# Performance work log

Measured on AMD Instinct MI355X. Metric: run time of the kernel, lower is better.

## Reference

```python
import jax, jax.numpy as jnp
import numpy as np

N, FEAT, D, H, C, FF, PH, E = 50000, 64, 128, 4, 32, 512, 256, 600000
LN_EPS = 1e-5
NEG_SLOPE = 0.2


def layer_norm(x, g, b):
    m = x.mean(-1, keepdims=True)
    v = ((x - m) ** 2).mean(-1, keepdims=True)
    return (x - m) * jax.lax.rsqrt(v + LN_EPS) * g + b


def gat_conv(x, edge_index, W, a_src, a_dst, bias):
    # PyG GATConv, concat=True, add_self_loops=True, negative_slope=0.2, eval mode.
    n = x.shape[0]
    h = (x @ W).reshape(n, H, C)                       # [N,H,C]
    al_s = jnp.einsum('nhc,hc->nh', h, a_src)          # [N,H]
    al_d = jnp.einsum('nhc,hc->nh', h, a_dst)
    loops = jnp.arange(n)
    src = jnp.concatenate([edge_index[0], loops])      # [E+N]
    dst = jnp.concatenate([edge_index[1], loops])
    alpha = jax.nn.leaky_relu(al_s[src] + al_d[dst], NEG_SLOPE)  # [E+N,H]
    amax = jax.lax.stop_gradient(jax.ops.segment_max(alpha, dst, num_segments=n))
    ex = jnp.exp(alpha - amax[dst])
    denom = jax.ops.segment_sum(ex, dst, num_segments=n)
    w = ex / denom[dst]                                # segment softmax over incoming edges
    msg = h[src] * w[:, :, None]                       # [E+N,H,C]
    out = jax.ops.segment_sum(msg, dst, num_segments=n).reshape(n, H * C)
    return out + bias


def encoder_layer(x, ei, W, a_s, a_d, b, W1, b1, W2, b2, g1, bt1, g2, bt2):
    h = gat_conv(x, ei, W, a_s, a_d, b)
    x = layer_norm(x + h, g1, bt1)
    f = jax.nn.relu(x @ W1 + b1) @ W2 + b2
    return layer_norm(x + f, g2, bt2)


def setup_inputs() -> dict:
    key = jax.random.key(0)
    ks = iter(jax.random.split(key, 64))
    rn = lambda shp, s=0.08: jax.random.normal(next(ks), shp, dtype=jnp.float32) * s
    d = {}
    d['x'] = jax.random.normal(next(ks), (N, FEAT), dtype=jnp.float32)
    d['edge_index'] = jax.random.randint(next(ks), (2, E), 0, N)
    d['virtual_edge_index'] = jax.random.randint(next(ks), (2, E), 0, N)
    d['Wp'] = rn((FEAT, D)); d['bp'] = jnp.zeros((D,))
    d['lnp_g'] = jnp.ones((D,)); d['lnp_b'] = jnp.zeros((D,))
    for p in ('v', 'r'):
        d[p + 'W'] = rn((2, D, D)); d[p + '_as'] = rn((2, H, C), 0.1); d[p + '_ad'] = rn((2, H, C), 0.1)
        d[p + '_b'] = jnp.zeros((2, D))
        d[p + 'W1'] = rn((2, D, FF)); d[p + 'b1'] = jnp.zeros((2, FF))
        d[p + 'W2'] = rn((2, FF, D)); d[p + 'b2'] = jnp.zeros((2, D))
        d[p + 'ln1g'] = jnp.ones((2, D)); d[p + 'ln1b'] = jnp.zeros((2, D))
        d[p + 'ln2g'] = jnp.ones((2, D)); d[p + 'ln2b'] = jnp.zeros((2, D))
    d['We1'] = rn((2 * D, PH)); d['be1'] = jnp.zeros((PH,))
    d['We2'] = rn((PH, 1)); d['be2'] = jnp.zeros((1,))
    return d


def reference(x, edge_index, virtual_edge_index, Wp, bp, lnp_g, lnp_b,
              vW, v_as, v_ad, v_b, vW1, vb1, vW2, vb2, vln1g, vln1b, vln2g, vln2b,
              rW, r_as, r_ad, r_b, rW1, rb1, rW2, rb2, rln1g, rln1b, rln2g, rln2b,
              We1, be1, We2, be2):
    # preprocessing
    h = layer_norm(jax.nn.relu(x @ Wp + bp), lnp_g, lnp_b)
    # virtual-link encoders
    for i in range(vW.shape[0]):
        h = encoder_layer(h, virtual_edge_index, vW[i], v_as[i], v_ad[i], v_b[i],
                          vW1[i], vb1[i], vW2[i], vb2[i], vln1g[i], vln1b[i], vln2g[i], vln2b[i])
    # real-link encoders
    for i in range(rW.shape[0]):
        h = encoder_layer(h, edge_index, rW[i], r_as[i], r_ad[i], r_b[i],
                          rW1[i], rb1[i], rW2[i], rb2[i], rln1g[i], rln1b[i], rln2g[i], rln2b[i])
    # edge predictor
    ef = jnp.concatenate([h[edge_index[0]], h[edge_index[1]]], axis=-1)  # [E,2D]
    flow = (jax.nn.relu(ef @ We1 + be1) @ We2 + be2)[:, 0]
    return jax.nn.relu(flow)
```

## Files before the change

kernel.cpp:

```cpp
#include <hip/hip_runtime.h>
#include <hip/hip_bf16.h>
#include <math.h>

#define NODES 50000
#define NFEAT 64
#define DIM 128
#define HEADS 4
#define CHC 32
#define FFDIM 512
#define PHDIM 256
#define NEDGE 600000
#define LN_EPS 1e-5f
#define SLOPE 0.2f

typedef __attribute__((ext_vector_type(8))) short bf16x8;
typedef __attribute__((ext_vector_type(4))) float f32x4;
typedef __attribute__((ext_vector_type(4))) unsigned short us4;

__device__ __forceinline__ unsigned short f2bf(float f) {
    __hip_bfloat16 h = __float2bfloat16(f);
    return reinterpret_cast<unsigned short&>(h);
}
__device__ __forceinline__ float bf2f(unsigned short u) {
    return __uint_as_float(((unsigned int)u) << 16);
}

__device__ __forceinline__ void ln_stats128(float val, float* red, float& mean, float& rstd) {
    float s1 = val, s2 = val * val;
#pragma unroll
    for (int off = 32; off > 0; off >>= 1) {
        s1 += __shfl_xor(s1, off, 64);
        s2 += __shfl_xor(s2, off, 64);
    }
    int wv = threadIdx.x >> 6;
    if ((threadIdx.x & 63) == 0) { red[wv * 2] = s1; red[wv * 2 + 1] = s2; }
    __syncthreads();
    float t1 = red[0] + red[2];
    float t2 = red[1] + red[3];
    mean = t1 * (1.f / 128.f);
    float var = t2 * (1.f / 128.f) - mean * mean;
    rstd = rsqrtf(var + LN_EPS);
}

__global__ void k_count(const int* __restrict__ dst, int* __restrict__ cnt) {
    int e = blockIdx.x * 256 + threadIdx.x;
    if (e < NEDGE) atomicAdd(&cnt[dst[e]], 1);
}

__global__ void k_scan(const int* __restrict__ deg, int* __restrict__ rp) {
    __shared__ int sh[1024];
    int t = threadIdx.x;
    const int per = (NODES + 1023) / 1024;
    int beg = t * per;
    int end = beg + per; if (end > NODES) end = NODES; if (beg > NODES) beg = NODES;
    int s = 0;
    for (int i = beg; i < end; i++) s += deg[i];
    sh[t] = s;
    __syncthreads();
    for (int off = 1; off < 1024; off <<= 1) {
        int v = (t >= off) ? sh[t - off] : 0;
        __syncthreads();
        sh[t] += v;
        __syncthreads();
    }
    int run = sh[t] - s;
    for (int i = beg; i < end; i++) { rp[i] = run; run += deg[i]; }
    if (t == 1023) rp[NODES] = sh[1023];
}

__global__ void k_fill(const int* __restrict__ ei, const int* __restrict__ rp,
                       int* __restrict__ cnt, int* __restrict__ ci) {
    int e = blockIdx.x * 256 + threadIdx.x;
    if (e < NEDGE) {
        int s = ei[e], d = ei[NEDGE + e];
        int pos = atomicAdd(&cnt[d], 1);
        ci[rp[d] + pos] = s;
    }
}

template <int KI, int NR>
__global__ void k_wcvt2(const float* __restrict__ in, unsigned short* __restrict__ oh,
                        unsigned short* __restrict__ ol) {
    int tid = blockIdx.x * 256 + threadIdx.x;
    int n = tid / KI, k = tid % KI;
    float w = in[k * NR + n];
    unsigned short h = f2bf(w);
    oh[tid] = h;
    ol[tid] = f2bf(w - bf2f(h));
}

__global__ void k_preprocess(const float* __restrict__ x0, const float* __restrict__ Wp,
                             const float* __restrict__ bp, const float* __restrict__ g,
                             const float* __restrict__ b, float* __restrict__ xout) {
    __shared__ float xr[NFEAT];
    __shared__ float red[4];
    int n = blockIdx.x;
    int j = threadIdx.x;
    if (j < NFEAT) xr[j] = x0[n * NFEAT + j];
    __syncthreads();
    float acc = bp[j];
#pragma unroll
    for (int k = 0; k < NFEAT; k++) acc += xr[k] * Wp[k * DIM + j];
    acc = fmaxf(acc, 0.f);
    float mean, rstd;
    ln_stats128(acc, red, mean, rstd);
    xout[n * DIM + j] = (acc - mean) * rstd * g[j] + b[j];
}

#define XS_STRIDE 136
#define HID_STRIDE 520
#define FB_STRIDE 132
#define MFMA_BF16 __builtin_amdgcn_mfma_f32_16x16x32_bf16

__global__ void k_xw_mfma(const float* __restrict__ x,
                          const unsigned short* __restrict__ Wh,
                          const unsigned short* __restrict__ Wl,
                          const float* __restrict__ a_s, const float* __restrict__ a_d,
                          float* __restrict__ hg, float* __restrict__ als,
                          float* __restrict__ ald) {
    __shared__ __align__(16) unsigned short xsh[32 * XS_STRIDE];
    __shared__ __align__(16) unsigned short xsl[32 * XS_STRIDE];
    int t = threadIdx.x;
    int n0 = blockIdx.x * 32;

#pragma unroll
    for (int jj = 0; jj < 4; jj++) {
        int v = t + jj * 256;
        int m = v >> 5, c4 = (v & 31) * 4;
        int node = n0 + m;
        float4 f;
        if (node < NODES) f = *(const float4*)(x + (size_t)node * DIM + c4);
        else { f.x = f.y = f.z = f.w = 0.f; }
        us4 uh = {f2bf(f.x), f2bf(f.y), f2bf(f.z), f2bf(f.w)};
        us4 ul = {f2bf(f.x - bf2f(uh.x)), f2bf(f.y - bf2f(uh.y)),
                  f2bf(f.z - bf2f(uh.z)), f2bf(f.w - bf2f(uh.w))};
        *(us4*)(xsh + m * XS_STRIDE + c4) = uh;
        *(us4*)(xsl + m * XS_STRIDE + c4) = ul;
    }
    __syncthreads();

    int wv = t >> 6, l = t & 63, lr = l & 15, lk = l >> 4;

    f32x4 acc[2][2];
#pragma unroll
    for (int mf = 0; mf < 2; mf++)
#pragma unroll
        for (int nf = 0; nf < 2; nf++) acc[mf][nf] = (f32x4){0.f, 0.f, 0.f, 0.f};
#pragma unroll
    for (int kk = 0; kk < 4; kk++) {
        int c = kk * 32 + lk * 8;
        bf16x8 a0h = *(const bf16x8*)(xsh + lr * XS_STRIDE + c);
        bf16x8 a0l = *(const bf16x8*)(xsl + lr * XS_STRIDE + c);
        bf16x8 a1h = *(const bf16x8*)(xsh + (16 + lr) * XS_STRIDE + c);
        bf16x8 a1l = *(const bf16x8*)(xsl + (16 + lr) * XS_STRIDE + c);
#pragma unroll
        for (int nf = 0; nf < 2; nf++) {
            int n = wv * 32 + nf * 16 + lr;
            bf16x8 bh = *(const bf16x8*)(Wh + (size_t)n * DIM + c);
            bf16x8 bl = *(const bf16x8*)(Wl + (size_t)n * DIM + c);
            acc[0][nf] = MFMA_BF16(a0h, bh, acc[0][nf], 0, 0, 0);
            acc[0][nf] = MFMA_BF16(a0l, bh, acc[0][nf], 0, 0, 0);
            acc[0][nf] = MFMA_BF16(a0h, bl, acc[0][nf], 0, 0, 0);
            acc[1][nf] = MFMA_BF16(a1h, bh, acc[1][nf], 0, 0, 0);
            acc[1][nf] = MFMA_BF16(a1l, bh, acc[1][nf], 0, 0, 0);
            acc[1][nf] = MFMA_BF16(a1h, bl, acc[1][nf], 0, 0, 0);
        }
    }

    float as0 = a_s[wv * 32 + lr], as1 = a_s[wv * 32 + 16 + lr];
    float ad0 = a_d[wv * 32 + lr], ad1 = a_d[wv * 32 + 16 + lr];
#pragma unroll
    for (int mf = 0; mf < 2; mf++) {
#pragma unroll
        for (int r = 0; r < 4; r++) {
            int m = mf * 16 + lk * 4 + r;
            int node = n0 + m;
            float v0 = acc[mf][0][r], v1 = acc[mf][1][r];
            if (node < NODES) {
                hg[(size_t)node * DIM + wv * 32 + lr] = v0;
                hg[(size_t)node * DIM + wv * 32 + 16 + lr] = v1;
            }
            float ps = v0 * as0 + v1 * as1;
            float pd = v0 * ad0 + v1 * ad1;
#pragma unroll
            for (int off = 8; off > 0; off >>= 1) {
                ps += __shfl_xor(ps, off, 64);
                pd += __shfl_xor(pd, off, 64);
            }
            if (lr == 0 && node < NODES) {
                als[node * HEADS + wv] = ps;
                ald[node * HEADS + wv] = pd;
            }
        }
    }
}

__global__ void k_agg(const float* __restrict__ x, const float* __restrict__ hg,
                      const float* __restrict__ als, const float* __restrict__ ald,
                      const int* __restrict__ rp, const int* __restrict__ ci,
                      const float* __restrict__ bias, const float* __restrict__ g,
                      const float* __restrict__ b, float* __restrict__ y) {
    __shared__ float red[4];
    int n = blockIdx.x, j = threadIdx.x, head = j >> 5;
    float aldn = ald[n * HEADS + head];
    float a0 = als[n * HEADS + head] + aldn;
    a0 = (a0 > 0.f) ? a0 : SLOPE * a0;
    float ex = __expf(a0);
    float den = ex;
    float acc = ex * hg[(size_t)n * DIM + j];
    int beg = rp[n], end = rp[n + 1];
    int e = beg;
    for (; e + 4 <= end; e += 4) {
        int s0 = ci[e], s1 = ci[e + 1], s2 = ci[e + 2], s3 = ci[e + 3];
        float av0 = als[s0 * HEADS + head] + aldn;
        float av1 = als[s1 * HEADS + head] + aldn;
        float av2 = als[s2 * HEADS + head] + aldn;
        float av3 = als[s3 * HEADS + head] + aldn;
        av0 = (av0 > 0.f) ? av0 : SLOPE * av0;
        av1 = (av1 > 0.f) ? av1 : SLOPE * av1;
        av2 = (av2 > 0.f) ? av2 : SLOPE * av2;
        av3 = (av3 > 0.f) ? av3 : SLOPE * av3;
        float e0 = __expf(av0), e1 = __expf(av1), e2 = __expf(av2), e3 = __expf(av3);
        float h0 = hg[(size_t)s0 * DIM + j];
        float h1 = hg[(size_t)s1 * DIM + j];
        float h2 = hg[(size_t)s2 * DIM + j];
        float h3 = hg[(size_t)s3 * DIM + j];
        den += (e0 + e1) + (e2 + e3);
        acc += e0 * h0 + e1 * h1 + e2 * h2 + e3 * h3;
    }
    for (; e < end; e++) {
        int s = ci[e];
        float av = als[s * HEADS + head] + aldn;
        av = (av > 0.f) ? av : SLOPE * av;
        float e2 = __expf(av);
        den += e2;
        acc += e2 * hg[(size_t)s * DIM + j];
    }
    float val = x[(size_t)n * DIM + j] + acc / den + bias[j];
    float mean, rstd;
    ln_stats128(val, red, mean, rstd);
    y[(size_t)n * DIM + j] = (val - mean) * rstd * g[j] + b[j];
}

#define TM 32

__global__ void k_ffn_mfma(
    const float* __restrict__ yin,
    const unsigned short* __restrict__ W1h, const unsigned short* __restrict__ W1l,
    const float* __restrict__ b1,
    const unsigned short* __restrict__ W2h, const unsigned short* __restrict__ W2l,
    const float* __restrict__ b2, const float* __restrict__ g,
    const float* __restrict__ b, float* __restrict__ xout) {
    __shared__ __align__(16) unsigned char smem[(2 * TM * XS_STRIDE + 2 * TM * HID_STRIDE) * 2];
    unsigned short* xsh = (unsigned short*)smem;
    unsigned short* xsl = xsh + TM * XS_STRIDE;
    unsigned short* hidh = xsl + TM * XS_STRIDE;
    unsigned short* hidl = hidh + TM * HID_STRIDE;
    float* fbuf = (float*)hidh;

    int t = threadIdx.x;
    int n0 = blockIdx.x * TM;

#pragma unroll
    for (int jj = 0; jj < 2; jj++) {
        int v = t + jj * 512;
        int m = v >> 5, c4 = (v & 31) * 4;
        int node = n0 + m;
        float4 f;
        if (node < NODES) f = *(const float4*)(yin + (size_t)node * DIM + c4);
        else { f.x = f.y = f.z = f.w = 0.f; }
        us4 uh = {f2bf(f.x), f2bf(f.y), f2bf(f.z), f2bf(f.w)};
        us4 ul = {f2bf(f.x - bf2f(uh.x)), f2bf(f.y - bf2f(uh.y)),
                  f2bf(f.z - bf2f(uh.z)), f2bf(f.w - bf2f(uh.w))};
        *(us4*)(xsh + m * XS_STRIDE + c4) = uh;
        *(us4*)(xsl + m * XS_STRIDE + c4) = ul;
    }
    __syncthreads();

    int wv = t >> 6, l = t & 63, lr = l & 15, lk = l >> 4;

    {
        f32x4 acc[2][4];
#pragma unroll
        for (int mf = 0; mf < 2; mf++)
#pragma unroll
            for (int nf = 0; nf < 4; nf++) acc[mf][nf] = (f32x4){0.f, 0.f, 0.f, 0.f};
#pragma unroll
        for (int kk = 0; kk < 4; kk++) {
            int c = kk * 32 + lk * 8;
            bf16x8 a0h = *(const bf16x8*)(xsh + lr * XS_STRIDE + c);
            bf16x8 a0l = *(const bf16x8*)(xsl + lr * XS_STRIDE + c);
            bf16x8 a1h = *(const bf16x8*)(xsh + (16 + lr) * XS_STRIDE + c);
            bf16x8 a1l = *(const bf16x8*)(xsl + (16 + lr) * XS_STRIDE + c);
#pragma unroll
            for (int nf = 0; nf < 4; nf++) {
                int n = wv * 64 + nf * 16 + lr;
                bf16x8 bh = *(const bf16x8*)(W1h + (size_t)n * DIM + c);
                bf16x8 bl = *(const bf16x8*)(W1l + (size_t)n * DIM + c);
                acc[0][nf] = MFMA_BF16(a0h, bh, acc[0][nf], 0, 0, 0);
                acc[0][nf] = MFMA_BF16(a0l, bh, acc[0][nf], 0, 0, 0);
                acc[0][nf] = MFMA_BF16(a0h, bl, acc[0][nf], 0, 0, 0);
                acc[1][nf] = MFMA_BF16(a1h, bh, acc[1][nf], 0, 0, 0);
                acc[1][nf] = MFMA_BF16(a1l, bh, acc[1][nf], 0, 0, 0);
                acc[1][nf] = MFMA_BF16(a1h, bl, acc[1][nf], 0, 0, 0);
            }
        }
#pragma unroll
        for (int nf = 0; nf < 4; nf++) {
            int n = wv * 64 + nf * 16 + lr;
            float bias = b1[n];
#pragma unroll
            for (int mf = 0; mf < 2; mf++)
#pragma unroll
                for (int r = 0; r < 4; r++) {
                    int m = mf * 16 + lk * 4 + r;
                    float val = fmaxf(acc[mf][nf][r] + bias, 0.f);
                    unsigned short h = f2bf(val);
                    hidh[m * HID_STRIDE + n] = h;
                    hidl[m * HID_STRIDE + n] = f2bf(val - bf2f(h));
                }
        }
    }
    __syncthreads();

    f32x4 acc2[2];
#pragma unroll
    for (int mf = 0; mf < 2; mf++) acc2[mf] = (f32x4){0.f, 0.f, 0.f, 0.f};
#pragma unroll
    for (int kk = 0; kk < 16; kk++) {
        int c = kk * 32 + lk * 8;
        bf16x8 a0h = *(const bf16x8*)(hidh + lr * HID_STRIDE + c);
        bf16x8 a0l = *(const bf16x8*)(hidl + lr * HID_STRIDE + c);
        bf16x8 a1h = *(const bf16x8*)(hidh + (16 + lr) * HID_STRIDE + c);
        bf16x8 a1l = *(const bf16x8*)(hidl + (16 + lr) * HID_STRIDE + c);
        int n = wv * 16 + lr;
        bf16x8 bh = *(const bf16x8*)(W2h + (size_t)n * FFDIM + c);
        bf16x8 bl = *(const bf16x8*)(W2l + (size_t)n * FFDIM + c);
        acc2[0] = MFMA_BF16(a0h, bh, acc2[0], 0, 0, 0);
        acc2[0] = MFMA_BF16(a0l, bh, acc2[0], 0, 0, 0);
        acc2[0] = MFMA_BF16(a0h, bl, acc2[0], 0, 0, 0);
        acc2[1] = MFMA_BF16(a1h, bh, acc2[1], 0, 0, 0);
        acc2[1] = MFMA_BF16(a1l, bh, acc2[1], 0, 0, 0);
        acc2[1] = MFMA_BF16(a1h, bl, acc2[1], 0, 0, 0);
    }
    __syncthreads();

    {
        int n = wv * 16 + lr;
        float bias = b2[n];
#pragma unroll
        for (int mf = 0; mf < 2; mf++)
#pragma unroll
            for (int r = 0; r < 4; r++) {
                int m = mf * 16 + lk * 4 + r;
                int node = n0 + m;
                float yv = (node < NODES) ? yin[(size_t)node * DIM + n] : 0.f;
                fbuf[m * FB_STRIDE + n] = acc2[mf][r] + bias + yv;
            }
    }
    __syncthreads();

    {
        int row = t >> 4, l16 = t & 15;
        float4 vv[2];
        float s1 = 0.f, s2 = 0.f;
#pragma unroll
        for (int q = 0; q < 2; q++) {
            vv[q] = *(float4*)(fbuf + row * FB_STRIDE + l16 * 8 + q * 4);
            s1 += vv[q].x + vv[q].y + vv[q].z + vv[q].w;
            s2 += vv[q].x * vv[q].x + vv[q].y * vv[q].y + vv[q].z * vv[q].z + vv[q].w * vv[q].w;
        }
#pragma unroll
        for (int off = 8; off > 0; off >>= 1) {
            s1 += __shfl_xor(s1, off, 64);
            s2 += __shfl_xor(s2, off, 64);
        }
        float mean = s1 * (1.f / 128.f);
        float var = s2 * (1.f / 128.f) - mean * mean;
        float rstd = rsqrtf(var + LN_EPS);
        int node = n0 + row;
        if (node < NODES) {
#pragma unroll
            for (int q = 0; q < 2; q++) {
                int c = l16 * 8 + q * 4;
                float4 gv = *(const float4*)(g + c);
                float4 bv = *(const float4*)(b + c);
                float4 o;
                o.x = (vv[q].x - mean) * rstd * gv.x + bv.x;
                o.y = (vv[q].y - mean) * rstd * gv.y + bv.y;
                o.z = (vv[q].z - mean) * rstd * gv.z + bv.z;
                o.w = (vv[q].w - mean) * rstd * gv.w + bv.w;
                *(float4*)(xout + (size_t)node * DIM + c) = o;
            }
        }
    }
}

#define TF 16
__global__ void k_pq(const float* __restrict__ h, const float* __restrict__ We1,
                     const float* __restrict__ be1, __hip_bfloat16* __restrict__ P,
                     __hip_bfloat16* __restrict__ Q) {
    __shared__ float xs[TF][DIM];
    int n0 = blockIdx.x * TF;
    int t = threadIdx.x;
    for (int i = t; i < TF * DIM; i += 256) {
        int e = i >> 7, k = i & 127;
        xs[e][k] = h[(size_t)(n0 + e) * DIM + k];
    }
    __syncthreads();
    float accP[TF], accQ[TF];
#pragma unroll
    for (int e = 0; e < TF; e++) { accP[e] = be1[t]; accQ[e] = 0.f; }
    for (int k = 0; k < DIM; k++) {
        float wp = We1[k * PHDIM + t];
        float wq = We1[(DIM + k) * PHDIM + t];
#pragma unroll
        for (int e = 0; e < TF; e++) {
            float xv = xs[e][k];
            accP[e] += xv * wp;
            accQ[e] += xv * wq;
        }
    }
#pragma unroll
    for (int e = 0; e < TF; e++) {
        P[(size_t)(n0 + e) * PHDIM + t] = __float2bfloat16(accP[e]);
        Q[(size_t)(n0 + e) * PHDIM + t] = __float2bfloat16(accQ[e]);
    }
}

__global__ void k_edge(const int* __restrict__ ei, const __hip_bfloat16* __restrict__ P,
                       const __hip_bfloat16* __restrict__ Q, const float* __restrict__ We2,
                       const float* __restrict__ be2, float* __restrict__ out) {
    int lane = threadIdx.x & 63;
    int wv = threadIdx.x >> 6;
    int e = blockIdx.x * 4 + wv;
    if (e >= NEDGE) return;
    float4 w2 = ((const float4*)We2)[lane];
    int s = ei[e], d = ei[NEDGE + e];
    uint2 pu = ((const uint2*)P)[(size_t)s * 64 + lane];
    uint2 qu = ((const uint2*)Q)[(size_t)d * 64 + lane];
    float p0 = __uint_as_float(pu.x << 16);
    float p1 = __uint_as_float(pu.x & 0xffff0000u);
    float p2 = __uint_as_float(pu.y << 16);
    float p3 = __uint_as_float(pu.y & 0xffff0000u);
    float q0 = __uint_as_float(qu.x << 16);
    float q1 = __uint_as_float(qu.x & 0xffff0000u);
    float q2 = __uint_as_float(qu.y << 16);
    float q3 = __uint_as_float(qu.y & 0xffff0000u);
    float acc = fmaxf(p0 + q0, 0.f) * w2.x + fmaxf(p1 + q1, 0.f) * w2.y +
                fmaxf(p2 + q2, 0.f) * w2.z + fmaxf(p3 + q3, 0.f) * w2.w;
#pragma unroll
    for (int off = 32; off > 0; off >>= 1) acc += __shfl_xor(acc, off, 64);
    if (lane == 0) out[e] = fmaxf(acc + be2[0], 0.f);
}

extern "C" void kernel_launch(void* const* d_in, const int* in_sizes, int n_in,
                              void* d_out, int out_size, void* d_ws, size_t ws_size,
                              hipStream_t stream) {
    const float* x0   = (const float*)d_in[0];
    const int*   eiR  = (const int*)d_in[1];
    const int*   eiV  = (const int*)d_in[2];
    const float* Wp   = (const float*)d_in[3];
    const float* bp   = (const float*)d_in[4];
    const float* lnpg = (const float*)d_in[5];
    const float* lnpb = (const float*)d_in[6];
    const float* vW   = (const float*)d_in[7];
    const float* v_as = (const float*)d_in[8];
    const float* v_ad = (const float*)d_in[9];
    const float* v_b  = (const float*)d_in[10];
    const float* vW1  = (const float*)d_in[11];
    const float* vb1  = (const float*)d_in[12];
    const float* vW2  = (const float*)d_in[13];
    const float* vb2  = (const float*)d_in[14];
    const float* vln1g = (const float*)d_in[15];
    const float* vln1b = (const float*)d_in[16];
    const float* vln2g = (const float*)d_in[17];
    const float* vln2b = (const float*)d_in[18];
    const float* rW   = (const float*)d_in[19];
    const float* r_as = (const float*)d_in[20];
    const float* r_ad = (const float*)d_in[21];
    const float* r_b  = (const float*)d_in[22];
    const float* rW1  = (const float*)d_in[23];
    const float* rb1  = (const float*)d_in[24];
    const float* rW2  = (const float*)d_in[25];
    const float* rb2  = (const float*)d_in[26];
    const float* rln1g = (const float*)d_in[27];
    const float* rln1b = (const float*)d_in[28];
    const float* rln2g = (const float*)d_in[29];
    const float* rln2b = (const float*)d_in[30];
    const float* We1  = (const float*)d_in[31];
    const float* be1  = (const float*)d_in[32];
    const float* We2  = (const float*)d_in[33];
    const float* be2  = (const float*)d_in[34];
    float* out = (float*)d_out;

    float* X   = (float*)d_ws;
    float* Y   = X + (size_t)NODES * DIM;
    float* HG  = Y + (size_t)NODES * DIM;
    float* ALS = HG + (size_t)NODES * DIM;
    float* ALD = ALS + (size_t)NODES * HEADS;
    __hip_bfloat16* Pb = (__hip_bfloat16*)(ALD + (size_t)NODES * HEADS);
    __hip_bfloat16* Qb = Pb + (size_t)NODES * PHDIM;
    unsigned short* WT = (unsigned short*)(Qb + (size_t)NODES * PHDIM);
    unsigned short* WXT = WT + (size_t)4 * 4 * 65536;
    int* rpV = (int*)(WXT + (size_t)4 * 2 * 16384);
    int* ciV = rpV + (NODES + 1);
    int* rpR = ciV + NEDGE;
    int* ciR = rpR + (NODES + 1);
    int* cnt = ciR + NEDGE;

    const int EB = (NEDGE + 255) / 256;

    hipMemsetAsync(cnt, 0, sizeof(int) * NODES, stream);
    k_count<<<EB, 256, 0, stream>>>(eiV + NEDGE, cnt);
    k_scan<<<1, 1024, 0, stream>>>(cnt, rpV);
    hipMemsetAsync(cnt, 0, sizeof(int) * NODES, stream);
    k_fill<<<EB, 256, 0, stream>>>(eiV, rpV, cnt, ciV);
    hipMemsetAsync(cnt, 0, sizeof(int) * NODES, stream);
    k_count<<<EB, 256, 0, stream>>>(eiR + NEDGE, cnt);
    k_scan<<<1, 1024, 0, stream>>>(cnt, rpR);
    hipMemsetAsync(cnt, 0, sizeof(int) * NODES, stream);
    k_fill<<<EB, 256, 0, stream>>>(eiR, rpR, cnt, ciR);

    for (int l = 0; l < 4; l++) {
        bool virt = (l < 2);
        int i = virt ? l : (l - 2);
        const float* W1 = (virt ? vW1 : rW1) + (size_t)i * DIM * FFDIM;
        const float* W2 = (virt ? vW2 : rW2) + (size_t)i * FFDIM * DIM;
        const float* W  = (virt ? vW : rW) + (size_t)i * DIM * DIM;
        unsigned short* base = WT + (size_t)l * 262144;
        k_wcvt2<DIM, FFDIM><<<256, 256, 0, stream>>>(W1, base, base + 65536);
        k_wcvt2<FFDIM, DIM><<<256, 256, 0, stream>>>(W2, base + 131072, base + 196608);
        unsigned short* bx = WXT + (size_t)l * 32768;
        k_wcvt2<DIM, DIM><<<64, 256, 0, stream>>>(W, bx, bx + 16384);
    }

    k_preprocess<<<NODES, 128, 0, stream>>>(x0, Wp, bp, lnpg, lnpb, X);

    for (int l = 0; l < 4; l++) {
        bool virt = (l < 2);
        int i = virt ? l : (l - 2);
        const float* As = (virt ? v_as : r_as) + (size_t)i * HEADS * CHC;
        const float* Ad = (virt ? v_ad : r_ad) + (size_t)i * HEADS * CHC;
        const float* Bb = (virt ? v_b : r_b) + (size_t)i * DIM;
        const float* B1 = (virt ? vb1 : rb1) + (size_t)i * FFDIM;
        const float* B2 = (virt ? vb2 : rb2) + (size_t)i * DIM;
        const float* G1 = (virt ? vln1g : rln1g) + (size_t)i * DIM;
        const float* B1n = (virt ? vln1b : rln1b) + (size_t)i * DIM;
        const float* G2 = (virt ? vln2g : rln2g) + (size_t)i * DIM;
        const float* B2n = (virt ? vln2b : rln2b) + (size_t)i * DIM;
        const int* rp = virt ? rpV : rpR;
        const int* ci = virt ? ciV : ciR;

        unsigned short* bx = WXT + (size_t)l * 32768;
        k_xw_mfma<<<(NODES + 31) / 32, 256, 0, stream>>>(X, bx, bx + 16384, As, Ad, HG, ALS, ALD);
        k_agg<<<NODES, 128, 0, stream>>>(X, HG, ALS, ALD, rp, ci, Bb, G1, B1n, Y);
        unsigned short* base = WT + (size_t)l * 262144;
        k_ffn_mfma<<<(NODES + TM - 1) / TM, 512, 0, stream>>>(
            Y, base, base + 65536, B1, base + 131072, base + 196608, B2, G2, B2n, X);
    }

    k_pq<<<NODES / TF, 256, 0, stream>>>(X, We1, be1, Pb, Qb);
    k_edge<<<(NEDGE + 3) / 4, 256, 0, stream>>>(eiR, Pb, Qb, We2, be2, out);
}
```

Baseline: 1.424 ms.

## Split FFN tile rows across twice as many waves in k_ffn_mfma

The FFN kernel now launches 1024 threads per block instead of 512, and each wave computes one 16-row half of the 32-row tile instead of both halves. This halves per-wave accumulator state and MFMA work, which adds waves for latency hiding. In exchange, every global weight fragment (W1, W2) is loaded by twice as many waves per block. The larger block may also limit how many blocks fit per CU.

```diff
diff --git a/kernel.cpp b/kernel.cpp
--- a/kernel.cpp
+++ b/kernel.cpp
@@ -261,10 +261,8 @@
     int t = threadIdx.x;
     int n0 = blockIdx.x * TM;
 
-#pragma unroll
-    for (int jj = 0; jj < 2; jj++) {
-        int v = t + jj * 512;
-        int m = v >> 5, c4 = (v & 31) * 4;
+    {
+        int m = t >> 5, c4 = (t & 31) * 4;
         int node = n0 + m;
         float4 f;
         if (node < NODES) f = *(const float4*)(yin + (size_t)node * DIM + c4);
@@ -278,100 +276,79 @@
     __syncthreads();
 
     int wv = t >> 6, l = t & 63, lr = l & 15, lk = l >> 4;
+    int mh = (wv & 1) * 16;
+    int cg = wv >> 1;
 
     {
-        f32x4 acc[2][4];
-#pragma unroll
-        for (int mf = 0; mf < 2; mf++)
-#pragma unroll
-            for (int nf = 0; nf < 4; nf++) acc[mf][nf] = (f32x4){0.f, 0.f, 0.f, 0.f};
+        f32x4 acc[4];
+#pragma unroll
+        for (int nf = 0; nf < 4; nf++) acc[nf] = (f32x4){0.f, 0.f, 0.f, 0.f};
 #pragma unroll
         for (int kk = 0; kk < 4; kk++) {
             int c = kk * 32 + lk * 8;
-            bf16x8 a0h = *(const bf16x8*)(xsh + lr * XS_STRIDE + c);
-            bf16x8 a0l = *(const bf16x8*)(xsl + lr * XS_STRIDE + c);
-            bf16x8 a1h = *(const bf16x8*)(xsh + (16 + lr) * XS_STRIDE + c);
-            bf16x8 a1l = *(const bf16x8*)(xsl + (16 + lr) * XS_STRIDE + c);
+            bf16x8 ah = *(const bf16x8*)(xsh + (mh + lr) * XS_STRIDE + c);
+            bf16x8 al = *(const bf16x8*)(xsl + (mh + lr) * XS_STRIDE + c);
 #pragma unroll
             for (int nf = 0; nf < 4; nf++) {
-                int n = wv * 64 + nf * 16 + lr;
+                int n = cg * 64 + nf * 16 + lr;
                 bf16x8 bh = *(const bf16x8*)(W1h + (size_t)n * DIM + c);
                 bf16x8 bl = *(const bf16x8*)(W1l + (size_t)n * DIM + c);
-                acc[0][nf] = MFMA_BF16(a0h, bh, acc[0][nf], 0, 0, 0);
-                acc[0][nf] = MFMA_BF16(a0l, bh, acc[0][nf], 0, 0, 0);
-                acc[0][nf] = MFMA_BF16(a0h, bl, acc[0][nf], 0, 0, 0);
-                acc[1][nf] = MFMA_BF16(a1h, bh, acc[1][nf], 0, 0, 0);
-                acc[1][nf] = MFMA_BF16(a1l, bh, acc[1][nf], 0, 0, 0);
-                acc[1][nf] = MFMA_BF16(a1h, bl, acc[1][nf], 0, 0, 0);
+                acc[nf] = MFMA_BF16(ah, bh, acc[nf], 0, 0, 0);
+                acc[nf] = MFMA_BF16(al, bh, acc[nf], 0, 0, 0);
+                acc[nf] = MFMA_BF16(ah, bl, acc[nf], 0, 0, 0);
             }
         }
 #pragma unroll
         for (int nf = 0; nf < 4; nf++) {
-            int n = wv * 64 + nf * 16 + lr;
+            int n = cg * 64 + nf * 16 + lr;
             float bias = b1[n];
 #pragma unroll
-            for (int mf = 0; mf < 2; mf++)
-#pragma unroll
-                for (int r = 0; r < 4; r++) {
-                    int m = mf * 16 + lk * 4 + r;
-                    float val = fmaxf(acc[mf][nf][r] + bias, 0.f);
-                    unsigned short h = f2bf(val);
-                    hidh[m * HID_STRIDE + n] = h;
-                    hidl[m * HID_STRIDE + n] = f2bf(val - bf2f(h));
-                }
-        }
-    }
-    __syncthreads();
-
-    f32x4 acc2[2];
-#pragma unroll
-    for (int mf = 0; mf < 2; mf++) acc2[mf] = (f32x4){0.f, 0.f, 0.f, 0.f};
+            for (int r = 0; r < 4; r++) {
+                int m = mh + lk * 4 + r;
+                float val = fmaxf(acc[nf][r] + bias, 0.f);
+                unsigned short h = f2bf(val);
+                hidh[m * HID_STRIDE + n] = h;
+                hidl[m * HID_STRIDE + n] = f2bf(val - bf2f(h));
+            }
+        }
+    }
+    __syncthreads();
+
+    f32x4 acc2 = (f32x4){0.f, 0.f, 0.f, 0.f};
 #pragma unroll
     for (int kk = 0; kk < 16; kk++) {
         int c = kk * 32 + lk * 8;
-        bf16x8 a0h = *(const bf16x8*)(hidh + lr * HID_STRIDE + c);
-        bf16x8 a0l = *(const bf16x8*)(hidl + lr * HID_STRIDE + c);
-        bf16x8 a1h = *(const bf16x8*)(hidh + (16 + lr) * HID_STRIDE + c);
-        bf16x8 a1l = *(const bf16x8*)(hidl + (16 + lr) * HID_STRIDE + c);
-        int n = wv * 16 + lr;
+        bf16x8 ah = *(const bf16x8*)(hidh + (mh + lr) * HID_STRIDE + c);
+        bf16x8 al = *(const bf16x8*)(hidl + (mh + lr) * HID_STRIDE + c);
+        int n = cg * 16 + lr;
         bf16x8 bh = *(const bf16x8*)(W2h + (size_t)n * FFDIM + c);
         bf16x8 bl = *(const bf16x8*)(W2l + (size_t)n * FFDIM + c);
-        acc2[0] = MFMA_BF16(a0h, bh, acc2[0], 0, 0, 0);
-        acc2[0] = MFMA_BF16(a0l, bh, acc2[0], 0, 0, 0);
-        acc2[0] = MFMA_BF16(a0h, bl, acc2[0], 0, 0, 0);
-        acc2[1] = MFMA_BF16(a1h, bh, acc2[1], 0, 0, 0);
-        acc2[1] = MFMA_BF16(a1l, bh, acc2[1], 0, 0, 0);
-        acc2[1] = MFMA_BF16(a1h, bl, acc2[1], 0, 0, 0);
+        acc2 = MFMA_BF16(ah, bh, acc2, 0, 0, 0);
+        acc2 = MFMA_BF16(al, bh, acc2, 0, 0, 0);
+        acc2 = MFMA_BF16(ah, bl, acc2, 0, 0, 0);
     }
     __syncthreads();
 
     {
-        int n = wv * 16 + lr;
+        int n = cg * 16 + lr;
         float bias = b2[n];
 #pragma unroll
-        for (int mf = 0; mf < 2; mf++)
-#pragma unroll
-            for (int r = 0; r < 4; r++) {
-                int m = mf * 16 + lk * 4 + r;
-                int node = n0 + m;
-                float yv = (node < NODES) ? yin[(size_t)node * DIM + n] : 0.f;
-                fbuf[m * FB_STRIDE + n] = acc2[mf][r] + bias + yv;
-            }
+        for (int r = 0; r < 4; r++) {
+            int m = mh + lk * 4 + r;
+            int node = n0 + m;
+            float yv = (node < NODES) ? yin[(size_t)node * DIM + n] : 0.f;
+            fbuf[m * FB_STRIDE + n] = acc2[r] + bias + yv;
+        }
     }
     __syncthreads();
 
     {
-        int row = t >> 4, l16 = t & 15;
-        float4 vv[2];
-        float s1 = 0.f, s2 = 0.f;
-#pragma unroll
-        for (int q = 0; q < 2; q++) {
-            vv[q] = *(float4*)(fbuf + row * FB_STRIDE + l16 * 8 + q * 4);
-            s1 += vv[q].x + vv[q].y + vv[q].z + vv[q].w;
-            s2 += vv[q].x * vv[q].x + vv[q].y * vv[q].y + vv[q].z * vv[q].z + vv[q].w * vv[q].w;
-        }
-#pragma unroll
-        for (int off = 8; off > 0; off >>= 1) {
+        int row = t >> 5, l32 = t & 31;
+        float4 vv = *(float4*)(fbuf + row * FB_STRIDE + l32 * 4);
+        float s1 = vv.x + vv.y + vv.z + vv.w;
+        float s2 = vv.x * vv.x + vv.y * vv.y + vv.z * vv.z + vv.w * vv.w;
+#pragma unroll
+        for (int off = 16; off > 0; off >>= 1) {
             s1 += __shfl_xor(s1, off, 64);
             s2 += __shfl_xor(s2, off, 64);
         }
@@ -380,18 +357,15 @@
         float rstd = rsqrtf(var + LN_EPS);
         int node = n0 + row;
         if (node < NODES) {
-#pragma unroll
-            for (int q = 0; q < 2; q++) {
-                int c = l16 * 8 + q * 4;
-                float4 gv = *(const float4*)(g + c);
-                float4 bv = *(const float4*)(b + c);
-                float4 o;
-                o.x = (vv[q].x - mean) * rstd * gv.x + bv.x;
-                o.y = (vv[q].y - mean) * rstd * gv.y + bv.y;
-                o.z = (vv[q].z - mean) * rstd * gv.z + bv.z;
-                o.w = (vv[q].w - mean) * rstd * gv.w + bv.w;
-                *(float4*)(xout + (size_t)node * DIM + c) = o;
-            }
+            int c = l32 * 4;
+            float4 gv = *(const float4*)(g + c);
+            float4 bv = *(const float4*)(b + c);
+            float4 o;
+            o.x = (vv.x - mean) * rstd * gv.x + bv.x;
+            o.y = (vv.y - mean) * rstd * gv.y + bv.y;
+            o.z = (vv.z - mean) * rstd * gv.z + bv.z;
+            o.w = (vv.w - mean) * rstd * gv.w + bv.w;
+            *(float4*)(xout + (size_t)node * DIM + c) = o;
         }
     }
 }
@@ -556,7 +530,7 @@
         k_xw_mfma<<<(NODES + 31) / 32, 256, 0, stream>>>(X, bx, bx + 16384, As, Ad, HG, ALS, ALD);
         k_agg<<<NODES, 128, 0, stream>>>(X, HG, ALS, ALD, rp, ci, Bb, G1, B1n, Y);
         unsigned short* base = WT + (size_t)l * 262144;
-        k_ffn_mfma<<<(NODES + TM - 1) / TM, 512, 0, stream>>>(
+        k_ffn_mfma<<<(NODES + TM - 1) / TM, 1024, 0, stream>>>(
             Y, base, base + 65536, B1, base + 131072, base + 196608, B2, G2, B2n, X);
     }
 
```

Result: slower. 1.780 ms (+25.0%).

## Compute edge predictor P/Q projection with split-bf16 MFMA instead of scalar FMA

Applied to the files above, without the earlier changes.

Replaces the scalar fp32 k_pq kernel with an MFMA kernel that computes both P and Q projections (N x 128 by 128 x 512) using a three-term hi/lo bf16 split to keep near-fp32 accuracy. A new conversion kernel pre-transposes and splits We1 into bf16 high/low buffers in the workspace. The intent is to move the 50000x128x512 GEMM off the vector ALUs onto matrix cores, at the cost of an extra weight conversion launch and strided per-element bf16 output stores.

```diff
diff --git a/kernel.cpp b/kernel.cpp
--- a/kernel.cpp
+++ b/kernel.cpp
@@ -84,6 +84,16 @@
     int tid = blockIdx.x * 256 + threadIdx.x;
     int n = tid / KI, k = tid % KI;
     float w = in[k * NR + n];
+    unsigned short h = f2bf(w);
+    oh[tid] = h;
+    ol[tid] = f2bf(w - bf2f(h));
+}
+
+__global__ void k_wcvt_pq(const float* __restrict__ We1, unsigned short* __restrict__ oh,
+                          unsigned short* __restrict__ ol) {
+    int tid = blockIdx.x * 256 + threadIdx.x;
+    int n = tid >> 7, k = tid & 127;
+    float w = (n < PHDIM) ? We1[k * PHDIM + n] : We1[(DIM + k) * PHDIM + (n - PHDIM)];
     unsigned short h = f2bf(w);
     oh[tid] = h;
     ol[tid] = f2bf(w - bf2f(h));
@@ -396,35 +406,75 @@
     }
 }
 
-#define TF 16
-__global__ void k_pq(const float* __restrict__ h, const float* __restrict__ We1,
-                     const float* __restrict__ be1, __hip_bfloat16* __restrict__ P,
-                     __hip_bfloat16* __restrict__ Q) {
-    __shared__ float xs[TF][DIM];
-    int n0 = blockIdx.x * TF;
+__global__ void k_pq_mfma(const float* __restrict__ x,
+                          const unsigned short* __restrict__ Wh,
+                          const unsigned short* __restrict__ Wl,
+                          const float* __restrict__ be1,
+                          __hip_bfloat16* __restrict__ P, __hip_bfloat16* __restrict__ Q) {
+    __shared__ __align__(16) unsigned short xsh[32 * XS_STRIDE];
+    __shared__ __align__(16) unsigned short xsl[32 * XS_STRIDE];
     int t = threadIdx.x;
-    for (int i = t; i < TF * DIM; i += 256) {
-        int e = i >> 7, k = i & 127;
-        xs[e][k] = h[(size_t)(n0 + e) * DIM + k];
-    }
-    __syncthreads();
-    float accP[TF], accQ[TF];
-#pragma unroll
-    for (int e = 0; e < TF; e++) { accP[e] = be1[t]; accQ[e] = 0.f; }
-    for (int k = 0; k < DIM; k++) {
-        float wp = We1[k * PHDIM + t];
-        float wq = We1[(DIM + k) * PHDIM + t];
-#pragma unroll
-        for (int e = 0; e < TF; e++) {
-            float xv = xs[e][k];
-            accP[e] += xv * wp;
-            accQ[e] += xv * wq;
-        }
-    }
-#pragma unroll
-    for (int e = 0; e < TF; e++) {
-        P[(size_t)(n0 + e) * PHDIM + t] = __float2bfloat16(accP[e]);
-        Q[(size_t)(n0 + e) * PHDIM + t] = __float2bfloat16(accQ[e]);
+    int n0 = blockIdx.x * 32;
+
+#pragma unroll
+    for (int jj = 0; jj < 4; jj++) {
+        int v = t + jj * 256;
+        int m = v >> 5, c4 = (v & 31) * 4;
+        int node = n0 + m;
+        float4 f;
+        if (node < NODES) f = *(const float4*)(x + (size_t)node * DIM + c4);
+        else { f.x = f.y = f.z = f.w = 0.f; }
+        us4 uh = {f2bf(f.x), f2bf(f.y), f2bf(f.z), f2bf(f.w)};
+        us4 ul = {f2bf(f.x - bf2f(uh.x)), f2bf(f.y - bf2f(uh.y)),
+                  f2bf(f.z - bf2f(uh.z)), f2bf(f.w - bf2f(uh.w))};
+        *(us4*)(xsh + m * XS_STRIDE + c4) = uh;
+        *(us4*)(xsl + m * XS_STRIDE + c4) = ul;
+    }
+    __syncthreads();
+
+    int wv = t >> 6, l = t & 63, lr = l & 15, lk = l >> 4;
+
+    f32x4 acc[2][8];
+#pragma unroll
+    for (int mf = 0; mf < 2; mf++)
+#pragma unroll
+        for (int nf = 0; nf < 8; nf++) acc[mf][nf] = (f32x4){0.f, 0.f, 0.f, 0.f};
+#pragma unroll
+    for (int kk = 0; kk < 4; kk++) {
+        int c = kk * 32 + lk * 8;
+        bf16x8 a0h = *(const bf16x8*)(xsh + lr * XS_STRIDE + c);
+        bf16x8 a0l = *(const bf16x8*)(xsl + lr * XS_STRIDE + c);
+        bf16x8 a1h = *(const bf16x8*)(xsh + (16 + lr) * XS_STRIDE + c);
+        bf16x8 a1l = *(const bf16x8*)(xsl + (16 + lr) * XS_STRIDE + c);
+#pragma unroll
+        for (int nf = 0; nf < 8; nf++) {
+            int n = wv * 128 + nf * 16 + lr;
+            bf16x8 bh = *(const bf16x8*)(Wh + (size_t)n * DIM + c);
+            bf16x8 bl = *(const bf16x8*)(Wl + (size_t)n * DIM + c);
+            acc[0][nf] = MFMA_BF16(a0h, bh, acc[0][nf], 0, 0, 0);
+            acc[0][nf] = MFMA_BF16(a0l, bh, acc[0][nf], 0, 0, 0);
+            acc[0][nf] = MFMA_BF16(a0h, bl, acc[0][nf], 0, 0, 0);
+            acc[1][nf] = MFMA_BF16(a1h, bh, acc[1][nf], 0, 0, 0);
+            acc[1][nf] = MFMA_BF16(a1l, bh, acc[1][nf], 0, 0, 0);
+            acc[1][nf] = MFMA_BF16(a1h, bl, acc[1][nf], 0, 0, 0);
+        }
+    }
+
+#pragma unroll
+    for (int nf = 0; nf < 8; nf++) {
+        int n = wv * 128 + nf * 16 + lr;
+        float bias = (n < PHDIM) ? be1[n] : 0.f;
+        __hip_bfloat16* dst = (n < PHDIM) ? P : Q;
+        int col = n & (PHDIM - 1);
+#pragma unroll
+        for (int mf = 0; mf < 2; mf++)
+#pragma unroll
+            for (int r = 0; r < 4; r++) {
+                int m = mf * 16 + lk * 4 + r;
+                int node = n0 + m;
+                if (node < NODES)
+                    dst[(size_t)node * PHDIM + col] = __float2bfloat16(acc[mf][nf][r] + bias);
+            }
     }
 }
 
@@ -503,7 +553,8 @@
     __hip_bfloat16* Qb = Pb + (size_t)NODES * PHDIM;
     unsigned short* WT = (unsigned short*)(Qb + (size_t)NODES * PHDIM);
     unsigned short* WXT = WT + (size_t)4 * 4 * 65536;
-    int* rpV = (int*)(WXT + (size_t)4 * 2 * 16384);
+    unsigned short* WPQ = WXT + (size_t)4 * 2 * 16384;
+    int* rpV = (int*)(WPQ + (size_t)2 * 65536);
     int* ciV = rpV + (NODES + 1);
     int* rpR = ciV + NEDGE;
     int* ciR = rpR + (NODES + 1);
@@ -534,6 +585,7 @@
         unsigned short* bx = WXT + (size_t)l * 32768;
         k_wcvt2<DIM, DIM><<<64, 256, 0, stream>>>(W, bx, bx + 16384);
     }
+    k_wcvt_pq<<<256, 256, 0, stream>>>(We1, WPQ, WPQ + 65536);
 
     k_preprocess<<<NODES, 128, 0, stream>>>(x0, Wp, bp, lnpg, lnpb, X);
 
@@ -560,6 +612,6 @@
             Y, base, base + 65536, B1, base + 131072, base + 196608, B2, G2, B2n, X);
     }
 
-    k_pq<<<NODES / TF, 256, 0, stream>>>(X, We1, be1, Pb, Qb);
+    k_pq_mfma<<<(NODES + 31) / 32, 256, 0, stream>>>(X, WPQ, WPQ + 65536, be1, Pb, Qb);
     k_edge<<<(NEDGE + 3) / 4, 256, 0, stream>>>(eiR, Pb, Qb, We2, be2, out);
 }
```

Measured after the change: 1.395 ms. 2.0% less time.
